# Performance work log

Hardware: AMD Instinct MI355X
Metric: run time of the kernel (lower is better)

The kernel has to match this reference:

```python
import jax, jax.numpy as jnp
import numpy as np

BETA = 0.25

def setup_inputs() -> dict:
    key = jax.random.key(0)
    k1, k2 = jax.random.split(key)
    z = jax.random.normal(k1, (16, 256, 32, 32), dtype=jnp.float32)
    # embedding initialized uniform(-1/ne, 1/ne) in the module; scale is immaterial for correctness
    ne = 8192
    codebook = jax.random.uniform(k2, (ne, 256), dtype=jnp.float32, minval=-1.0 / ne, maxval=1.0 / ne)
    return {"z": z, "codebook": codebook}


def reference(z, codebook):
    # z: [B, C, H, W] channel-first -> channel-last [B, H, W, C]
    z_cl = jnp.transpose(z, (0, 2, 3, 1))
    # distance (up to a constant ||z||^2 term, as in the original):
    # d = ||e||^2 - 2 <z, e>, shape [B, H, W, NE]
    d = jnp.sum(codebook ** 2, axis=1) - 2.0 * jnp.einsum('bhwd,nd->bhwn', z_cl, codebook)
    index = jnp.argmin(d, axis=-1)                      # [B, H, W]
    z_q = codebook[index]                               # [B, H, W, C] gather
    # commitment + codebook losses with straight-through
    loss = jnp.mean((jax.lax.stop_gradient(z_q) - z_cl) ** 2) \
         + BETA * jnp.mean((z_q - jax.lax.stop_gradient(z_cl)) ** 2)
    z_q_st = z_cl + jax.lax.stop_gradient(z_q - z_cl)   # straight-through estimator
    z_q_cf = jnp.transpose(z_q_st, (0, 3, 1, 2))        # back to channel-first [B, C, H, W]
    return z_q_cf, index, loss
```

## Files before the change

kernel.cpp:

```cpp
#include <hip/hip_runtime.h>
#include <float.h>

#define NPIX 16384
#define NE   8192
#define KD   256
#define HW   1024
#define BCHW 262144
#define NT   8
#define DELTA 2.5e-4f
#define KMASK 0xFFFFE000u

typedef __attribute__((ext_vector_type(8))) short short8;
typedef __attribute__((ext_vector_type(4))) short short4v;
typedef __attribute__((ext_vector_type(4))) float f32x4;
typedef __attribute__((ext_vector_type(4))) unsigned int u32x4;
typedef unsigned long long u64;
typedef unsigned int u32;

__device__ __forceinline__ u32 fkey(float f) {
    u32 u = __float_as_uint(f);
    return u ^ ((u >> 31) ? 0xFFFFFFFFu : 0x80000000u);
}
__device__ __forceinline__ short bf16rne(float f) {
    u32 u = __float_as_uint(f);
    u += 0x7FFFu + ((u >> 16) & 1u);
    return (short)(u >> 16);
}
__device__ __forceinline__ float kval(u32 pk) {
    return __uint_as_float(pk & KMASK);
}

#define GLDS(gp, lp) __builtin_amdgcn_global_load_lds( \
    (const __attribute__((address_space(1))) void*)(gp), \
    (__attribute__((address_space(3))) void*)(lp), 16, 0, 0)

__global__ void vq_prep(const float* __restrict__ cb, short* __restrict__ eh,
                        float* __restrict__ e2) {
    const int row  = (blockIdx.x * 256 + threadIdx.x) >> 6;
    const int lane = threadIdx.x & 63;
    const f32x4 v = *(const f32x4*)(cb + (size_t)row * KD + lane * 4);
    short4v h;
    h[0] = bf16rne(v[0]); h[1] = bf16rne(v[1]);
    h[2] = bf16rne(v[2]); h[3] = bf16rne(v[3]);
    *(short4v*)(eh + (size_t)row * KD + lane * 4) = h;
    float s = v[0]*v[0] + v[1]*v[1] + v[2]*v[2] + v[3]*v[3];
    #pragma unroll
    for (int m = 1; m < 64; m <<= 1) s += __shfl_xor(s, m);
    if (lane == 0) e2[row] = s;
}

__global__ void vq_zh(const float* __restrict__ z, short* __restrict__ zh) {
    __shared__ float ts[64][65];
    const int b   = blockIdx.z;
    const int k0  = blockIdx.y * 64;
    const int hw0 = blockIdx.x * 64;
    const int tid = threadIdx.x;
    const int pl  = tid & 63, kk = tid >> 6;
    #pragma unroll
    for (int i = 0; i < 16; ++i) {
        const int k = kk + 4 * i;
        ts[k][pl] = z[b * BCHW + (k0 + k) * HW + hw0 + pl];
    }
    __syncthreads();
    const int tx = tid & 15, ty = tid >> 4;
    #pragma unroll
    for (int j = 0; j < 4; ++j) {
        const int p = ty + 16 * j;
        short4v v;
        #pragma unroll
        for (int q = 0; q < 4; ++q) v[q] = bf16rne(ts[tx * 4 + q][p]);
        *(short4v*)(zh + (size_t)(b * HW + hw0 + p) * KD + k0 + tx * 4) = v;
    }
}

__global__ __launch_bounds__(512, 2) void vq_gemm(
    const short* __restrict__ zh, const short* __restrict__ eh,
    u32* __restrict__ best4)
{
    __shared__ short Bs[4][4096];

    const int tid  = threadIdx.x;
    const int lane = tid & 63;
    const int w    = tid >> 6;
    const int wm   = w >> 1, wn = w & 1;
    const int lr   = lane & 15;
    const int p0   = blockIdx.x * 128;
    const int nb0  = blockIdx.y * (NT * 128);

    const int sr = lane >> 2;
    const int ss = (lane & 3) ^ ((sr >> 1) & 3);
    const int q   = lane >> 4;
    const int rsw = (lr >> 1) & 3;

    u32 b1[2][4], b2[2][4];
    #pragma unroll
    for (int m = 0; m < 2; ++m)
        #pragma unroll
        for (int r = 0; r < 4; ++r) { b1[m][r] = 0xFFFFFFFFu; b2[m][r] = 0xFFFFFFFFu; }

    short8 afr[2][8];
    #pragma unroll
    for (int m = 0; m < 2; ++m) {
        const size_t rowb = (size_t)(p0 + wm * 32 + m * 16 + lr) * KD;
        #pragma unroll
        for (int ks = 0; ks < 8; ++ks)
            afr[m][ks] = *(const short8*)(zh + rowb + ks * 32 + q * 8);
    }
    asm volatile("s_waitcnt vmcnt(0)" ::: "memory");

    #define STAGEB(nt_, t_, buf_) do {                                         \
        const int k0_ = (t_) * 32;                                             \
        const int n0_ = nb0 + (nt_) * 128;                                     \
        GLDS(eh + (size_t)(n0_ + w * 16 + sr) * KD + k0_ + ss * 8,             \
             &Bs[buf_][w * 512]);                                              \
    } while (0)

    f32x4 acc[2][4];

    STAGEB(0, 0, 0);
    STAGEB(0, 1, 1);

    #pragma unroll 1
    for (int nt = 0; nt < NT; ++nt) {
        const bool lastnt = (nt == NT - 1);
        #pragma unroll
        for (int t = 0; t < 8; ++t) {
            if (lastnt && t == 7) asm volatile("s_waitcnt vmcnt(0)" ::: "memory");
            else                  asm volatile("s_waitcnt vmcnt(1)" ::: "memory");
            __builtin_amdgcn_sched_barrier(0);
            __builtin_amdgcn_s_barrier();

            if (t < 6)        { STAGEB(nt, t + 2, (t + 2) & 3); }
            else if (!lastnt) { STAGEB(nt + 1, t - 6, (t - 6) & 3); }

            if (t == 0) {
                #pragma unroll
                for (int m = 0; m < 2; ++m)
                    #pragma unroll
                    for (int nf = 0; nf < 4; ++nf)
                        acc[m][nf] = (f32x4){0.f, 0.f, 0.f, 0.f};
            }

            short8 bfv[4];
            #pragma unroll
            for (int nf = 0; nf < 4; ++nf) {
                const int row = wn * 64 + nf * 16 + lr;
                bfv[nf] = *(const short8*)&Bs[t & 3][row * 32 + ((q ^ rsw) * 8)];
            }
            #pragma unroll
            for (int m = 0; m < 2; ++m)
                #pragma unroll
                for (int nf = 0; nf < 4; ++nf)
                    acc[m][nf] = __builtin_amdgcn_mfma_f32_16x16x32_bf16(
                        afr[m][t], bfv[nf], acc[m][nf], 0, 0, 0);

            if (t == 7) {
                const u32 nbase = (u32)(nb0 + nt * 128 + wn * 64 + lr);
                #pragma unroll
                for (int m = 0; m < 2; ++m) {
                    #pragma unroll
                    for (int r = 0; r < 4; ++r) {
                        u32 pk0 = (__float_as_uint(0.0625f - acc[m][0][r]) & KMASK) | (nbase);
                        u32 pk1 = (__float_as_uint(0.0625f - acc[m][1][r]) & KMASK) | (nbase + 16u);
                        u32 pk2 = (__float_as_uint(0.0625f - acc[m][2][r]) & KMASK) | (nbase + 32u);
                        u32 pk3 = (__float_as_uint(0.0625f - acc[m][3][r]) & KMASK) | (nbase + 48u);
                        const u32 lo01 = min(pk0, pk1), hi01 = max(pk0, pk1);
                        const u32 lo23 = min(pk2, pk3), hi23 = max(pk2, pk3);
                        const u32 m1 = min(lo01, lo23);
                        const u32 m2 = min(max(lo01, lo23), min(hi01, hi23));
                        const u32 nb1 = min(b1[m][r], m1);
                        const u32 nb2 = min(max(b1[m][r], m1), min(b2[m][r], m2));
                        b1[m][r] = nb1; b2[m][r] = nb2;
                    }
                }
            }
        }
    }
    #undef STAGEB

    const int g = lane >> 4;
    const int hs = blockIdx.y * 2 + wn;
    #pragma unroll
    for (int m = 0; m < 2; ++m) {
        #pragma unroll
        for (int r = 0; r < 4; ++r) {
            u32 a = b1[m][r], b = b2[m][r];
            u32 o[4];
            #pragma unroll
            for (int j = 0; j < 4; ++j) {
                u32 mm = a;
                #pragma unroll
                for (int msk = 1; msk < 16; msk <<= 1)
                    mm = min(mm, (u32)__shfl_xor((int)mm, msk));
                o[j] = mm;
                if (a == mm) { a = b; b = 0xFFFFFFFFu; }
            }
            if (lr == 0) {
                const int prow = p0 + wm * 32 + m * 16 + g * 4 + r;
                u32x4 ov; ov[0] = o[0]; ov[1] = o[1]; ov[2] = o[2]; ov[3] = o[3];
                *(u32x4*)&best4[((size_t)prow * 16 + hs) * 4] = ov;
            }
        }
    }
}

__global__ __launch_bounds__(256) void vq_exact(
    const float* __restrict__ z, const float* __restrict__ cb,
    const float* __restrict__ e2, const u32* __restrict__ best4,
    u64* __restrict__ final_)
{
    __shared__ float zb[16][260];
    __shared__ u32 work[1024];
    __shared__ u32 scans[256];
    __shared__ int nwork, nscan;

    const int tid = threadIdx.x;
    const int g0  = blockIdx.x * 16;
    const int bb  = g0 >> 10, hw0 = g0 & 1023;
    const int pix = tid >> 4;
    const int hsx = tid & 15;

    if (tid == 0) { nwork = 0; nscan = 0; }
    __syncthreads();

    const u32x4 kv = *(const u32x4*)&best4[((size_t)(g0 + pix) * 16 + hsx) * 4];
    const u32 lmin = min(min(kv[0], kv[1]), min(kv[2], kv[3]));
    u32 mn = lmin;
    #pragma unroll
    for (int m = 1; m < 16; m <<= 1) mn = min(mn, (u32)__shfl_xor((int)mn, m));
    const float thr = kval(mn) + DELTA;
    const int c4 = (kval(kv[0]) <= thr ? 1 : 0) + (kval(kv[1]) <= thr ? 1 : 0)
                 + (kval(kv[2]) <= thr ? 1 : 0) + (kval(kv[3]) <= thr ? 1 : 0);
    int cnt = c4;
    #pragma unroll
    for (int m = 1; m < 16; m <<= 1) cnt += __shfl_xor(cnt, m);
    const int susp = (c4 == 4) ? 1 : 0;
    int anysusp = susp;
    #pragma unroll
    for (int m = 1; m < 16; m <<= 1) anysusp += __shfl_xor(anysusp, m);

    if (cnt == 1 && anysusp == 0) {
        if (lmin == mn) final_[g0 + pix] = (u64)(mn & 8191u);
    } else {
        if (c4 > 0) {
            const int base = atomicAdd(&nwork, c4);
            int k = 0;
            #pragma unroll
            for (int j = 0; j < 4; ++j)
                if (kval(kv[j]) <= thr)
                    work[base + (k++)] = ((u32)pix << 13) | (kv[j] & 8191u);
        }
        if (susp) scans[atomicAdd(&nscan, 1)] = ((u32)pix << 4) | (u32)hsx;
    }
    __syncthreads();
    const int nw = nwork, ns = nscan;
    if (nw == 0 && ns == 0) return;

    #pragma unroll
    for (int i = 0; i < 16; ++i) {
        const int idx = i * 256 + tid;
        const int c = idx >> 4, px = idx & 15;
        zb[px][c] = z[(size_t)bb * BCHW + (size_t)c * HW + hw0 + px];
    }
    __syncthreads();

    for (int i = tid; i < nw; i += 256) {
        const u32 e = work[i];
        const int px = (int)(e >> 13), n = (int)(e & 8191u);
        const float* er = cb + (size_t)n * KD;
        float acc = 0.f;
        #pragma unroll 4
        for (int k = 0; k < KD; k += 4) {
            const f32x4 zv = *(const f32x4*)&zb[px][k];
            const f32x4 ev = *(const f32x4*)(er + k);
            acc += zv[0]*ev[0] + zv[1]*ev[1] + zv[2]*ev[2] + zv[3]*ev[3];
        }
        const float s = 0.5f * e2[n] - acc;
        atomicMin(&final_[g0 + px], ((u64)fkey(s) << 32) | (u32)n);
    }

    for (int si = 0; si < ns; ++si) {
        const u32 e = scans[si];
        const int px = (int)(e >> 4), hx = (int)(e & 15u);
        u64 bku = ~0ULL;
        #pragma unroll
        for (int h = 0; h < 2; ++h) {
            const int ci = tid + h * 256;
            const int n = (hx >> 1) * 1024 + (ci >> 6) * 128
                        + (hx & 1) * 64 + (ci & 63);
            const float* er = cb + (size_t)n * KD;
            float acc = 0.f;
            #pragma unroll 4
            for (int k = 0; k < KD; k += 4) {
                const f32x4 zv = *(const f32x4*)&zb[px][k];
                const f32x4 ev = *(const f32x4*)(er + k);
                acc += zv[0]*ev[0] + zv[1]*ev[1] + zv[2]*ev[2] + zv[3]*ev[3];
            }
            const float s = 0.5f * e2[n] - acc;
            const u64 pk = ((u64)fkey(s) << 32) | (u32)n;
            bku = min(bku, pk);
        }
        #pragma unroll
        for (int m = 1; m < 64; m <<= 1) {
            const u64 o = (u64)__shfl_xor((long long)bku, m);
            bku = min(bku, o);
        }
        if ((tid & 63) == 0) atomicMin(&final_[g0 + px], bku);
    }
}

__global__ __launch_bounds__(256) void vq_out_kernel(
    const float* __restrict__ z, const float* __restrict__ cb,
    const u64* __restrict__ final_, float* __restrict__ out,
    float* __restrict__ idxf, float* __restrict__ loss)
{
    __shared__ float zq[32][257];
    __shared__ int   nidx[32];

    const int tid = threadIdx.x;
    const int p0  = blockIdx.x * 32;
    const int bb  = p0 >> 10;
    const int hw0 = p0 & 1023;

    if (tid < 32) {
        const int n = (int)((u32)final_[p0 + tid] & 8191u);
        nidx[tid] = n;
        idxf[p0 + tid] = (float)n;
    }
    __syncthreads();

    {
        const int r = tid >> 3, i = tid & 7;
        const float* src = cb + (size_t)nidx[r] * KD;
        #pragma unroll
        for (int j = 0; j < 8; ++j) {
            const int col = i * 4 + j * 32;
            const f32x4 v = *(const f32x4*)(src + col);
            zq[r][col + 0] = v[0]; zq[r][col + 1] = v[1];
            zq[r][col + 2] = v[2]; zq[r][col + 3] = v[3];
        }
    }
    __syncthreads();

    const int p4 = (tid & 7) * 4;
    const int cg = tid >> 3;
    float ls = 0.f;
    #pragma unroll
    for (int ii = 0; ii < 8; ++ii) {
        const int c = cg + 32 * ii;
        const size_t e = (size_t)bb * BCHW + (size_t)c * HW + hw0 + p4;
        const f32x4 zv = *(const f32x4*)(z + e);
        f32x4 v;
        v[0] = zq[p4 + 0][c]; v[1] = zq[p4 + 1][c];
        v[2] = zq[p4 + 2][c]; v[3] = zq[p4 + 3][c];
        *(f32x4*)(out + e) = v;
        const float d0 = v[0] - zv[0], d1 = v[1] - zv[1];
        const float d2 = v[2] - zv[2], d3 = v[3] - zv[3];
        ls += d0 * d0 + d1 * d1 + d2 * d2 + d3 * d3;
    }
    #pragma unroll
    for (int m = 1; m < 64; m <<= 1) ls += __shfl_xor(ls, m);
    if ((tid & 63) == 0) atomicAdd(loss, ls * (1.25f / 4194304.f));
}

extern "C" void kernel_launch(void* const* d_in, const int* in_sizes, int n_in,
                              void* d_out, int out_size, void* d_ws, size_t ws_size,
                              hipStream_t stream) {
    const float* z  = (const float*)d_in[0];
    const float* cb = (const float*)d_in[1];
    float* out  = (float*)d_out;
    float* idxf = out + 4194304;
    float* loss = out + 4210688;
    char* ob = (char*)d_out;
    short* zh    = (short*)ob;
    short* eh    = (short*)(ob + 8388608);
    u32*   best4 = (u32*)(ob + 12582912);

    char* ws = (char*)d_ws;
    u64*   final_ = (u64*)ws;
    float* e2     = (float*)(ws + 131072);

    hipMemsetAsync(final_, 0xFF, 131072, stream);
    hipMemsetAsync(loss, 0, 4, stream);

    vq_prep<<<2048, 256, 0, stream>>>(cb, eh, e2);
    vq_zh<<<dim3(16, 4, 16), 256, 0, stream>>>(z, zh);
    vq_gemm<<<dim3(NPIX / 128, NE / (NT * 128)), 512, 0, stream>>>(zh, eh, best4);
    vq_exact<<<NPIX / 16, 256, 0, stream>>>(z, cb, e2, best4, final_);
    vq_out_kernel<<<NPIX / 32, 256, 0, stream>>>(z, cb, final_, out, idxf, loss);
}
```

Baseline: 191.6 us.

## Fuse exact rescoring into output kernel with shared-memory argmin

Merges the exact-distance rescoring kernel into the output/loss kernel. Each block handles 32 pixels and keeps the per-pixel best candidate in shared memory instead of a global buffer, so the global final buffer, its memset and one launch go away. The z tile staged in LDS is reused for the loss, so z is no longer reloaded from global memory. In exchange each block needs more shared memory (zb, zq and larger work lists), which may lower occupancy, and the z tile is now loaded even when no rescoring is needed.

```diff
diff --git a/kernel.cpp b/kernel.cpp
--- a/kernel.cpp
+++ b/kernel.cpp
@@ -204,65 +204,84 @@
     }
 }
 
-__global__ __launch_bounds__(256) void vq_exact(
+__global__ __launch_bounds__(256) void vq_out_kernel(
     const float* __restrict__ z, const float* __restrict__ cb,
     const float* __restrict__ e2, const u32* __restrict__ best4,
-    u64* __restrict__ final_)
+    float* __restrict__ out, float* __restrict__ idxf,
+    float* __restrict__ loss)
 {
-    __shared__ float zb[16][260];
-    __shared__ u32 work[1024];
-    __shared__ u32 scans[256];
-    __shared__ int nwork, nscan;
+    __shared__ float zb[32][260];
+    __shared__ float zq[32][257];
+    __shared__ u64  sfinal[32];
+    __shared__ int  nidx[32];
+    __shared__ u32  work[2048];
+    __shared__ u32  scans[512];
+    __shared__ int  nwork, nscan;
 
     const int tid = threadIdx.x;
-    const int g0  = blockIdx.x * 16;
-    const int bb  = g0 >> 10, hw0 = g0 & 1023;
-    const int pix = tid >> 4;
-    const int hsx = tid & 15;
+    const int p0  = blockIdx.x * 32;
+    const int bb  = p0 >> 10, hw0 = p0 & 1023;
 
     if (tid == 0) { nwork = 0; nscan = 0; }
-    __syncthreads();
-
-    const u32x4 kv = *(const u32x4*)&best4[((size_t)(g0 + pix) * 16 + hsx) * 4];
-    const u32 lmin = min(min(kv[0], kv[1]), min(kv[2], kv[3]));
-    u32 mn = lmin;
-    #pragma unroll
-    for (int m = 1; m < 16; m <<= 1) mn = min(mn, (u32)__shfl_xor((int)mn, m));
-    const float thr = kval(mn) + DELTA;
-    const int c4 = (kval(kv[0]) <= thr ? 1 : 0) + (kval(kv[1]) <= thr ? 1 : 0)
-                 + (kval(kv[2]) <= thr ? 1 : 0) + (kval(kv[3]) <= thr ? 1 : 0);
-    int cnt = c4;
-    #pragma unroll
-    for (int m = 1; m < 16; m <<= 1) cnt += __shfl_xor(cnt, m);
-    const int susp = (c4 == 4) ? 1 : 0;
-    int anysusp = susp;
-    #pragma unroll
-    for (int m = 1; m < 16; m <<= 1) anysusp += __shfl_xor(anysusp, m);
-
-    if (cnt == 1 && anysusp == 0) {
-        if (lmin == mn) final_[g0 + pix] = (u64)(mn & 8191u);
-    } else {
-        if (c4 > 0) {
-            const int base = atomicAdd(&nwork, c4);
-            int k = 0;
-            #pragma unroll
-            for (int j = 0; j < 4; ++j)
-                if (kval(kv[j]) <= thr)
-                    work[base + (k++)] = ((u32)pix << 13) | (kv[j] & 8191u);
-        }
-        if (susp) scans[atomicAdd(&nscan, 1)] = ((u32)pix << 4) | (u32)hsx;
-    }
-    __syncthreads();
+    if (tid < 32) sfinal[tid] = ~0ULL;
+    __syncthreads();
+
+    {
+        const int pix = tid >> 3;
+        const int hp  = (tid & 7) * 2;
+        const u32* src = &best4[((size_t)(p0 + pix) * 16 + hp) * 4];
+        const u32x4 kv0 = *(const u32x4*)(src);
+        const u32x4 kv1 = *(const u32x4*)(src + 4);
+        u32 lmin = min(min(kv0[0], kv0[1]), min(kv0[2], kv0[3]));
+        lmin = min(lmin, min(min(kv1[0], kv1[1]), min(kv1[2], kv1[3])));
+        u32 mn = lmin;
+        #pragma unroll
+        for (int m = 1; m < 8; m <<= 1) mn = min(mn, (u32)__shfl_xor((int)mn, m));
+        const float thr = kval(mn) + DELTA;
+        int c8 = 0;
+        #pragma unroll
+        for (int j = 0; j < 4; ++j) c8 += (kval(kv0[j]) <= thr) ? 1 : 0;
+        #pragma unroll
+        for (int j = 0; j < 4; ++j) c8 += (kval(kv1[j]) <= thr) ? 1 : 0;
+        int cnt = c8;
+        #pragma unroll
+        for (int m = 1; m < 8; m <<= 1) cnt += __shfl_xor(cnt, m);
+        const int s0 = (kval(kv0[3]) <= thr) ? 1 : 0;
+        const int s1 = (kval(kv1[3]) <= thr) ? 1 : 0;
+        int anysusp = s0 + s1;
+        #pragma unroll
+        for (int m = 1; m < 8; m <<= 1) anysusp += __shfl_xor(anysusp, m);
+
+        if (cnt == 1 && anysusp == 0) {
+            if (lmin == mn) sfinal[pix] = (u64)(mn & 8191u);
+        } else {
+            if (c8 > 0) {
+                const int base = atomicAdd(&nwork, c8);
+                int k = 0;
+                #pragma unroll
+                for (int j = 0; j < 4; ++j)
+                    if (kval(kv0[j]) <= thr)
+                        work[base + (k++)] = ((u32)pix << 13) | (kv0[j] & 8191u);
+                #pragma unroll
+                for (int j = 0; j < 4; ++j)
+                    if (kval(kv1[j]) <= thr)
+                        work[base + (k++)] = ((u32)pix << 13) | (kv1[j] & 8191u);
+            }
+            if (s0) scans[atomicAdd(&nscan, 1)] = ((u32)pix << 4) | (u32)hp;
+            if (s1) scans[atomicAdd(&nscan, 1)] = ((u32)pix << 4) | (u32)(hp + 1);
+        }
+    }
+    __syncthreads();
+
+    #pragma unroll
+    for (int i = 0; i < 32; ++i) {
+        const int idx = i * 256 + tid;
+        const int c = idx >> 5, px = idx & 31;
+        zb[px][c] = z[(size_t)bb * BCHW + (size_t)c * HW + hw0 + px];
+    }
+    __syncthreads();
+
     const int nw = nwork, ns = nscan;
-    if (nw == 0 && ns == 0) return;
-
-    #pragma unroll
-    for (int i = 0; i < 16; ++i) {
-        const int idx = i * 256 + tid;
-        const int c = idx >> 4, px = idx & 15;
-        zb[px][c] = z[(size_t)bb * BCHW + (size_t)c * HW + hw0 + px];
-    }
-    __syncthreads();
 
     for (int i = tid; i < nw; i += 256) {
         const u32 e = work[i];
@@ -276,7 +295,7 @@
             acc += zv[0]*ev[0] + zv[1]*ev[1] + zv[2]*ev[2] + zv[3]*ev[3];
         }
         const float s = 0.5f * e2[n] - acc;
-        atomicMin(&final_[g0 + px], ((u64)fkey(s) << 32) | (u32)n);
+        atomicMin(&sfinal[px], ((u64)fkey(s) << 32) | (u32)n);
     }
 
     for (int si = 0; si < ns; ++si) {
@@ -305,25 +324,12 @@
             const u64 o = (u64)__shfl_xor((long long)bku, m);
             bku = min(bku, o);
         }
-        if ((tid & 63) == 0) atomicMin(&final_[g0 + px], bku);
-    }
-}
-
-__global__ __launch_bounds__(256) void vq_out_kernel(
-    const float* __restrict__ z, const float* __restrict__ cb,
-    const u64* __restrict__ final_, float* __restrict__ out,
-    float* __restrict__ idxf, float* __restrict__ loss)
-{
-    __shared__ float zq[32][257];
-    __shared__ int   nidx[32];
-
-    const int tid = threadIdx.x;
-    const int p0  = blockIdx.x * 32;
-    const int bb  = p0 >> 10;
-    const int hw0 = p0 & 1023;
+        if ((tid & 63) == 0) atomicMin(&sfinal[px], bku);
+    }
+    __syncthreads();
 
     if (tid < 32) {
-        const int n = (int)((u32)final_[p0 + tid] & 8191u);
+        const int n = (int)((u32)sfinal[tid] & 8191u);
         nidx[tid] = n;
         idxf[p0 + tid] = (float)n;
     }
@@ -349,13 +355,12 @@
     for (int ii = 0; ii < 8; ++ii) {
         const int c = cg + 32 * ii;
         const size_t e = (size_t)bb * BCHW + (size_t)c * HW + hw0 + p4;
-        const f32x4 zv = *(const f32x4*)(z + e);
         f32x4 v;
         v[0] = zq[p4 + 0][c]; v[1] = zq[p4 + 1][c];
         v[2] = zq[p4 + 2][c]; v[3] = zq[p4 + 3][c];
         *(f32x4*)(out + e) = v;
-        const float d0 = v[0] - zv[0], d1 = v[1] - zv[1];
-        const float d2 = v[2] - zv[2], d3 = v[3] - zv[3];
+        const float d0 = v[0] - zb[p4 + 0][c], d1 = v[1] - zb[p4 + 1][c];
+        const float d2 = v[2] - zb[p4 + 2][c], d3 = v[3] - zb[p4 + 3][c];
         ls += d0 * d0 + d1 * d1 + d2 * d2 + d3 * d3;
     }
     #pragma unroll
@@ -376,16 +381,12 @@
     short* eh    = (short*)(ob + 8388608);
     u32*   best4 = (u32*)(ob + 12582912);
 
-    char* ws = (char*)d_ws;
-    u64*   final_ = (u64*)ws;
-    float* e2     = (float*)(ws + 131072);
-
-    hipMemsetAsync(final_, 0xFF, 131072, stream);
+    float* e2 = (float*)d_ws;
+
     hipMemsetAsync(loss, 0, 4, stream);
 
     vq_prep<<<2048, 256, 0, stream>>>(cb, eh, e2);
     vq_zh<<<dim3(16, 4, 16), 256, 0, stream>>>(z, zh);
     vq_gemm<<<dim3(NPIX / 128, NE / (NT * 128)), 512, 0, stream>>>(zh, eh, best4);
-    vq_exact<<<NPIX / 16, 256, 0, stream>>>(z, cb, e2, best4, final_);
-    vq_out_kernel<<<NPIX / 32, 256, 0, stream>>>(z, cb, final_, out, idxf, loss);
-}
+    vq_out_kernel<<<NPIX / 32, 256, 0, stream>>>(z, cb, e2, best4, out, idxf, loss);
+}
```

Result: faster. 179.7 us (-6.2%).
